# Kernel optimization log

Hardware: AMD Instinct MI355X
Metric: run time of the kernel (lower is better)

## Reference

```python
import jax, jax.numpy as jnp
from jax import lax
import numpy as np

T, D, H, E, K = 4096, 1024, 2048, 8, 2

def setup_inputs() -> dict:
    key = jax.random.key(0)
    ks = jax.random.split(key, 5)
    x = jax.random.normal(ks[0], (T, D), dtype=jnp.float32)
    weights = jax.random.uniform(ks[1], (T, K), dtype=jnp.float32)
    indices = jax.random.randint(ks[2], (T, K), 0, E, dtype=jnp.int64)
    # GatedMLP params (bias=False): fc1 weight [2H, D], fc2 weight [D, H], stacked over experts
    W1 = jax.random.normal(ks[3], (E, 2 * H, D), dtype=jnp.float32) * 0.02
    W2 = jax.random.normal(ks[4], (E, D, H), dtype=jnp.float32) * 0.02
    return {"x": x, "weights": weights, "indices": indices, "W1": W1, "W2": W2}

def reference(x, weights, indices, W1, W2):
    # Combine per-token routing weights into a per-(token, expert) weight matrix.
    # Tokens not routed to expert e get weight 0, so the dense per-expert GatedMLP
    # weighted-sum is mathematically identical to the gather->MLP->scatter-add loop.
    onehot = jax.nn.one_hot(indices, E, dtype=weights.dtype)        # [T, K, E]
    w_te = jnp.einsum('tke,tk->et', onehot, weights)                # [E, T]

    def body(y, carry):
        W1e, W2e, we = carry                                        # [2H,D], [D,H], [T]
        h = x @ W1e.T                                               # [T, 2H]
        u, gate = jnp.split(h, 2, axis=-1)                          # [T, H] each
        out = (u * jax.nn.silu(gate)) @ W2e.T                       # [T, D]
        return y + out * we[:, None], None

    y, _ = lax.scan(body, jnp.zeros_like(x), (W1, W2, w_te))
    return y
```

## Files before the change

kernel.cpp:

```cpp
#include <hip/hip_runtime.h>
#include <stdint.h>

#define T_TOK 4096
#define D_DIM 1024
#define H_DIM 2048
#define E_EXP 8
#define K_TOP 2
#define NTK   (T_TOK * K_TOP)
#define MT1 256
#define MAXT1 48

typedef short bf16x8 __attribute__((ext_vector_type(8)));
typedef float f32x4  __attribute__((ext_vector_type(4)));

#define MINI(a, b) ((a) < (b) ? (a) : (b))
#define MFMA_BF16 __builtin_amdgcn_mfma_f32_16x16x32_bf16

__device__ __forceinline__ unsigned short f2bf(float f) {
  unsigned u = __float_as_uint(f);
  u += 0x7fffu + ((u >> 16) & 1u);
  return (unsigned short)(u >> 16);
}

#define GLDS16(gp, lp)                                                        \
  __builtin_amdgcn_global_load_lds(                                           \
      (const __attribute__((address_space(1))) void*)(gp),                    \
      (__attribute__((address_space(3))) void*)(lp), 16, 0, 0)



__global__ __launch_bounds__(256) void k_route_count(const int* __restrict__ idx,
                                                     int* __restrict__ meta) {
  __shared__ int h[E_EXP];
  int tid = threadIdx.x;
  if (tid < E_EXP) h[tid] = 0;
  __syncthreads();
  int i = blockIdx.x * 256 + tid;
  atomicAdd(&h[idx[i] & (E_EXP - 1)], 1);
  __syncthreads();
  if (tid < E_EXP) atomicAdd(&meta[tid], h[tid]);
}

__global__ __launch_bounds__(64) void k_route_plan(int* __restrict__ meta) {
  if (threadIdx.x) return;
  int off = 0, nt = 0;
  for (int e = 0; e < E_EXP; ++e) {
    int c = meta[e];
    meta[8 + e]  = off;
    meta[16 + e] = off;
    for (int r = 0; r < c; r += MT1) {
      meta[32 + nt]  = e;
      meta[80 + nt]  = off + r;
      meta[128 + nt] = MINI(MT1, c - r);
      ++nt;
    }
    off += c;
  }
  meta[24] = nt;
}

__global__ __launch_bounds__(256) void k_route_scatter(const int* __restrict__ idx,
                                                       const float* __restrict__ w,
                                                       int* __restrict__ meta,
                                                       int* __restrict__ rows,
                                                       float* __restrict__ wv) {
  __shared__ int h[E_EXP], base[E_EXP];
  int tid = threadIdx.x;
  if (tid < E_EXP) h[tid] = 0;
  __syncthreads();
  int i = blockIdx.x * 256 + tid;
  int e = idx[i] & (E_EXP - 1);
  int r = atomicAdd(&h[e], 1);
  __syncthreads();
  if (tid < E_EXP) base[tid] = atomicAdd(&meta[16 + tid], h[tid]);
  __syncthreads();
  int p = base[e] + r;
  rows[p] = i >> 1;
  wv[p]   = w[i];
}

#define NX8   (T_TOK * D_DIM / 8)
#define NW18  (E_EXP * 2 * H_DIM * D_DIM / 8)
#define NW28  (E_EXP * D_DIM * H_DIM / 8)
#define NCVT8 (NX8 + NW18 + NW28)

__global__ __launch_bounds__(256) void k_cvt8(const float* __restrict__ x,
                                              const float* __restrict__ W1,
                                              const float* __restrict__ W2,
                                              unsigned short* __restrict__ xb,
                                              unsigned short* __restrict__ W1b,
                                              unsigned short* __restrict__ W2b) {
  long gid = (long)blockIdx.x * 256 + threadIdx.x;
  const float* src;
  unsigned short* dst;
  long i;
  if (gid < NX8) {
    src = x; dst = xb; i = gid;
  } else if (gid < NX8 + NW18) {
    src = W1; dst = W1b; i = gid - NX8;
  } else if (gid < NCVT8) {
    src = W2; dst = W2b; i = gid - (NX8 + NW18);
  } else return;
  float4 a = ((const float4*)src)[2 * i];
  float4 b = ((const float4*)src)[2 * i + 1];
  uint4 o;
  o.x = f2bf(a.x) | ((unsigned)f2bf(a.y) << 16);
  o.y = f2bf(a.z) | ((unsigned)f2bf(a.w) << 16);
  o.z = f2bf(b.x) | ((unsigned)f2bf(b.y) << 16);
  o.w = f2bf(b.z) | ((unsigned)f2bf(b.w) << 16);
  ((uint4*)dst)[i] = o;
}

__global__ __launch_bounds__(256, 2) void k_gemm1(
    const unsigned short* __restrict__ xb,
    const unsigned short* __restrict__ W1b,
    const int* __restrict__ meta,
    const int* __restrict__ rows,
    const float* __restrict__ wv,
    unsigned short* __restrict__ act) {
  int nt = meta[24];
  int bid = blockIdx.x;
  int xcd = bid & 7, jj = bid >> 3;
  int y   = jj & 31;
  int tb  = ((jj >> 5) << 3) + xcd;
  if (tb >= nt) return;
  int e     = meta[32 + tb];
  int r0    = meta[80 + tb];
  int valid = meta[128 + tb];
  int n0    = y << 6;

  __shared__ unsigned short lA[256 * 64];
  __shared__ unsigned short lB1[64 * 64];
  __shared__ unsigned short lB2[64 * 64];
  __shared__ float sw[256];

  int tid = threadIdx.x;
  int wave = tid >> 6, lane = tid & 63;

  sw[tid] = wv[r0 + MINI(tid, valid - 1)];

  const unsigned short* w1e = W1b + (size_t)e * (4096 * 1024);

  const unsigned short *pA[8], *pB1[2], *pB2[2];
#pragma unroll
  for (int it = 0; it < 8; ++it) {
    int c = it * 256 + tid;
    int r = c >> 3, cc = c & 7;
    int g = cc ^ (r & 7);
    int tok = rows[r0 + MINI(r, valid - 1)];
    pA[it] = xb + (size_t)tok * 1024 + g * 8;
  }
#pragma unroll
  for (int it = 0; it < 2; ++it) {
    int c = it * 256 + tid;
    int r = c >> 3, cc = c & 7;
    int g = cc ^ (r & 7);
    pB1[it] = w1e + (size_t)(n0 + r) * 1024 + g * 8;
    pB2[it] = w1e + (size_t)(2048 + n0 + r) * 1024 + g * 8;
  }

  f32x4 zero = {0.f, 0.f, 0.f, 0.f};
  f32x4 au[4][4], ag[4][4];
#pragma unroll
  for (int i = 0; i < 4; ++i)
#pragma unroll
    for (int j = 0; j < 4; ++j) { au[i][j] = zero; ag[i][j] = zero; }

  int mb = wave * 64;
  int fr = lane & 15, q = lane >> 4;

  for (int k0 = 0; k0 < 1024; k0 += 64) {
    __syncthreads();
#pragma unroll
    for (int it = 0; it < 8; ++it)
      GLDS16(pA[it] + k0, &lA[(it * 256 + wave * 64) * 8]);
#pragma unroll
    for (int it = 0; it < 2; ++it) {
      int lb = (it * 256 + wave * 64) * 8;
      GLDS16(pB1[it] + k0, &lB1[lb]);
      GLDS16(pB2[it] + k0, &lB2[lb]);
    }
    __syncthreads();
#pragma unroll
    for (int kk = 0; kk < 2; ++kk) {
      int co = (((kk << 2) + q) ^ (fr & 7)) * 8 + fr * 64;
      bf16x8 a[4];
#pragma unroll
      for (int i = 0; i < 4; ++i)
        a[i] = *(const bf16x8*)&lA[(mb + i * 16) * 64 + co];
#pragma unroll
      for (int j = 0; j < 4; ++j) {
        bf16x8 bu = *(const bf16x8*)&lB1[(j * 16) * 64 + co];
        bf16x8 bg = *(const bf16x8*)&lB2[(j * 16) * 64 + co];
#pragma unroll
        for (int i = 0; i < 4; ++i) {
          au[i][j] = MFMA_BF16(a[i], bu, au[i][j], 0, 0, 0);
          ag[i][j] = MFMA_BF16(a[i], bg, ag[i][j], 0, 0, 0);
        }
      }
    }
  }

#pragma unroll
  for (int i = 0; i < 4; ++i) {
#pragma unroll
    for (int reg = 0; reg < 4; ++reg) {
      int lm = mb + i * 16 + q * 4 + reg;
      if (lm < valid) {
        float wrow = sw[lm];
        size_t orow = (size_t)(r0 + lm) * 2048;
#pragma unroll
        for (int j = 0; j < 4; ++j) {
          float u = au[i][j][reg];
          float g = ag[i][j][reg];
          float s = g / (1.f + __expf(-g));
          act[orow + (n0 + j * 16 + fr)] = f2bf(u * s * wrow);
        }
      }
    }
  }
}

__global__ __launch_bounds__(256, 2) void k_gemm2(
    const unsigned short* __restrict__ act,
    const unsigned short* __restrict__ W2b,
    const int* __restrict__ meta,
    const int* __restrict__ rows,
    float* __restrict__ out) {
  int nt = meta[24];
  int bid = blockIdx.x;
  int xcd = bid & 7, jj = bid >> 3;
  int y   = jj & 7;
  int tb  = ((jj >> 3) << 3) + xcd;
  if (tb >= nt) return;
  int e     = meta[32 + tb];
  int r0    = meta[80 + tb];
  int valid = meta[128 + tb];
  int n0    = y << 7;

  __shared__ unsigned short lA[256 * 64];
  __shared__ unsigned short lB[128 * 64];
  __shared__ int st[256];

  int tid = threadIdx.x;
  int wave = tid >> 6, lane = tid & 63;
  st[tid] = rows[r0 + MINI(tid, valid - 1)];

  const unsigned short* w2e = W2b + (size_t)e * (1024 * 2048);

  const unsigned short *pA[8], *pB[4];
#pragma unroll
  for (int it = 0; it < 8; ++it) {
    int c = it * 256 + tid;
    int r = c >> 3, cc = c & 7;
    int g = cc ^ (r & 7);
    pA[it] = act + (size_t)(r0 + MINI(r, valid - 1)) * 2048 + g * 8;
  }
#pragma unroll
  for (int it = 0; it < 4; ++it) {
    int c = it * 256 + tid;
    int r = c >> 3, cc = c & 7;
    int g = cc ^ (r & 7);
    pB[it] = w2e + (size_t)(n0 + r) * 2048 + g * 8;
  }

  f32x4 zero = {0.f, 0.f, 0.f, 0.f};
  f32x4 acc[4][8];
#pragma unroll
  for (int i = 0; i < 4; ++i)
#pragma unroll
    for (int j = 0; j < 8; ++j) acc[i][j] = zero;

  int mb = wave * 64;
  int fr = lane & 15, q = lane >> 4;

  for (int k0 = 0; k0 < 2048; k0 += 64) {
    __syncthreads();
#pragma unroll
    for (int it = 0; it < 8; ++it)
      GLDS16(pA[it] + k0, &lA[(it * 256 + wave * 64) * 8]);
#pragma unroll
    for (int it = 0; it < 4; ++it)
      GLDS16(pB[it] + k0, &lB[(it * 256 + wave * 64) * 8]);
    __syncthreads();
#pragma unroll
    for (int kk = 0; kk < 2; ++kk) {
      int co = (((kk << 2) + q) ^ (fr & 7)) * 8 + fr * 64;
      bf16x8 a[4];
#pragma unroll
      for (int i = 0; i < 4; ++i)
        a[i] = *(const bf16x8*)&lA[(mb + i * 16) * 64 + co];
#pragma unroll
      for (int j = 0; j < 8; ++j) {
        bf16x8 b = *(const bf16x8*)&lB[(j * 16) * 64 + co];
#pragma unroll
        for (int i = 0; i < 4; ++i)
          acc[i][j] = MFMA_BF16(a[i], b, acc[i][j], 0, 0, 0);
      }
    }
  }

#pragma unroll
  for (int i = 0; i < 4; ++i) {
#pragma unroll
    for (int reg = 0; reg < 4; ++reg) {
      int lm = mb + i * 16 + q * 4 + reg;
      if (lm < valid) {
        int tok = st[lm];
        float* op = out + (size_t)tok * 1024;
#pragma unroll
        for (int j = 0; j < 8; ++j)
          atomicAdd(&op[n0 + j * 16 + fr], acc[i][j][reg]);
      }
    }
  }
}

extern "C" void kernel_launch(void* const* d_in, const int* in_sizes, int n_in,
                              void* d_out, int out_size, void* d_ws, size_t ws_size,
                              hipStream_t stream) {
  const float* x  = (const float*)d_in[0];
  const float* w  = (const float*)d_in[1];
  const int*  idx = (const int*)d_in[2];
  const float* W1 = (const float*)d_in[3];
  const float* W2 = (const float*)d_in[4];
  float* out = (float*)d_out;

  char* ws = (char*)d_ws;
  unsigned short* W1b = (unsigned short*)(ws);
  unsigned short* W2b = (unsigned short*)(ws + 67108864);
  unsigned short* xb  = (unsigned short*)(ws + 100663296);
  unsigned short* act = (unsigned short*)(ws + 109051904);
  int*   rows = (int*)(ws + 142606336);
  float* wv   = (float*)(ws + 142639104);
  int*   meta = (int*)(ws + 142671872);

  hipMemsetAsync(d_out, 0, (size_t)out_size * sizeof(float), stream);
  hipMemsetAsync(meta, 0, 1024, stream);

  k_cvt8<<<(NCVT8 + 255) / 256, 256, 0, stream>>>(x, W1, W2, xb, W1b, W2b);
  k_route_count<<<32, 256, 0, stream>>>(idx, meta);
  k_route_plan<<<1, 64, 0, stream>>>(meta);
  k_route_scatter<<<32, 256, 0, stream>>>(idx, w, meta, rows, wv);

  k_gemm1<<<MAXT1 * 32, 256, 0, stream>>>(xb, W1b, meta, rows, wv, act);
  k_gemm2<<<MAXT1 * 8, 256, 0, stream>>>(act, W2b, meta, rows, out);
}
```

Before: 460.6 us.

## Overlap W2 conversion and output zeroing with gemm1; fuse route count into cvt

Result: faster. 423.0 us (-8.2%).

```diff
diff --git a/kernel.cpp b/kernel.cpp
--- a/kernel.cpp
+++ b/kernel.cpp
@@ -28,17 +28,44 @@
       (__attribute__((address_space(3))) void*)(lp), 16, 0, 0)
 
 
-
-__global__ __launch_bounds__(256) void k_route_count(const int* __restrict__ idx,
-                                                     int* __restrict__ meta) {
-  __shared__ int h[E_EXP];
+#define NX8   (T_TOK * D_DIM / 8)
+#define NW18  (E_EXP * 2 * H_DIM * D_DIM / 8)
+#define NW28  (E_EXP * D_DIM * H_DIM / 8)
+#define PRE_CVT_BLKS ((NX8 + NW18) / 256)
+#define PRE_BLKS (PRE_CVT_BLKS + 32)
+
+__global__ __launch_bounds__(256) void k_pre(const float* __restrict__ x,
+                                             const float* __restrict__ W1,
+                                             const int* __restrict__ idx,
+                                             unsigned short* __restrict__ xb,
+                                             unsigned short* __restrict__ W1b,
+                                             int* __restrict__ meta) {
+  int bid = blockIdx.x;
   int tid = threadIdx.x;
-  if (tid < E_EXP) h[tid] = 0;
-  __syncthreads();
-  int i = blockIdx.x * 256 + tid;
-  atomicAdd(&h[idx[i] & (E_EXP - 1)], 1);
-  __syncthreads();
-  if (tid < E_EXP) atomicAdd(&meta[tid], h[tid]);
+  if (bid >= PRE_CVT_BLKS) {
+    __shared__ int h[E_EXP];
+    if (tid < E_EXP) h[tid] = 0;
+    __syncthreads();
+    int i = (bid - PRE_CVT_BLKS) * 256 + tid;
+    atomicAdd(&h[idx[i] & (E_EXP - 1)], 1);
+    __syncthreads();
+    if (tid < E_EXP) atomicAdd(&meta[tid], h[tid]);
+    return;
+  }
+  long gid = (long)bid * 256 + tid;
+  const float* src;
+  unsigned short* dst;
+  long i;
+  if (gid < NX8) { src = x; dst = xb; i = gid; }
+  else           { src = W1; dst = W1b; i = gid - NX8; }
+  float4 a = ((const float4*)src)[2 * i];
+  float4 b = ((const float4*)src)[2 * i + 1];
+  uint4 o;
+  o.x = f2bf(a.x) | ((unsigned)f2bf(a.y) << 16);
+  o.y = f2bf(a.z) | ((unsigned)f2bf(a.w) << 16);
+  o.z = f2bf(b.x) | ((unsigned)f2bf(b.y) << 16);
+  o.w = f2bf(b.z) | ((unsigned)f2bf(b.w) << 16);
+  ((uint4*)dst)[i] = o;
 }
 
 __global__ __launch_bounds__(64) void k_route_plan(int* __restrict__ meta) {
@@ -79,37 +106,10 @@
   wv[p]   = w[i];
 }
 
-#define NX8   (T_TOK * D_DIM / 8)
-#define NW18  (E_EXP * 2 * H_DIM * D_DIM / 8)
-#define NW28  (E_EXP * D_DIM * H_DIM / 8)
-#define NCVT8 (NX8 + NW18 + NW28)
-
-__global__ __launch_bounds__(256) void k_cvt8(const float* __restrict__ x,
-                                              const float* __restrict__ W1,
-                                              const float* __restrict__ W2,
-                                              unsigned short* __restrict__ xb,
-                                              unsigned short* __restrict__ W1b,
-                                              unsigned short* __restrict__ W2b) {
-  long gid = (long)blockIdx.x * 256 + threadIdx.x;
-  const float* src;
-  unsigned short* dst;
-  long i;
-  if (gid < NX8) {
-    src = x; dst = xb; i = gid;
-  } else if (gid < NX8 + NW18) {
-    src = W1; dst = W1b; i = gid - NX8;
-  } else if (gid < NCVT8) {
-    src = W2; dst = W2b; i = gid - (NX8 + NW18);
-  } else return;
-  float4 a = ((const float4*)src)[2 * i];
-  float4 b = ((const float4*)src)[2 * i + 1];
-  uint4 o;
-  o.x = f2bf(a.x) | ((unsigned)f2bf(a.y) << 16);
-  o.y = f2bf(a.z) | ((unsigned)f2bf(a.w) << 16);
-  o.z = f2bf(b.x) | ((unsigned)f2bf(b.y) << 16);
-  o.w = f2bf(b.z) | ((unsigned)f2bf(b.w) << 16);
-  ((uint4*)dst)[i] = o;
-}
+#define G1_TILES (MAXT1 * 32)
+#define CVW2_BLK 1024
+#define ZOUT_BLK 64
+#define G1_GRID  (G1_TILES + CVW2_BLK + ZOUT_BLK)
 
 __global__ __launch_bounds__(256, 2) void k_gemm1(
     const unsigned short* __restrict__ xb,
@@ -117,12 +117,40 @@
     const int* __restrict__ meta,
     const int* __restrict__ rows,
     const float* __restrict__ wv,
-    unsigned short* __restrict__ act) {
+    unsigned short* __restrict__ act,
+    const float* __restrict__ W2,
+    unsigned short* __restrict__ W2b,
+    float* __restrict__ out) {
+  int bid = blockIdx.x;
+  int tid = threadIdx.x;
+
+  if (bid >= G1_TILES) {
+    int xb2 = bid - G1_TILES;
+    if (xb2 < CVW2_BLK) {
+      long g0 = (long)xb2 * 256 + tid;
+      for (long i = g0; i < NW28; i += (long)CVW2_BLK * 256) {
+        float4 a = ((const float4*)W2)[2 * i];
+        float4 b = ((const float4*)W2)[2 * i + 1];
+        uint4 o;
+        o.x = f2bf(a.x) | ((unsigned)f2bf(a.y) << 16);
+        o.y = f2bf(a.z) | ((unsigned)f2bf(a.w) << 16);
+        o.z = f2bf(b.x) | ((unsigned)f2bf(b.y) << 16);
+        o.w = f2bf(b.z) | ((unsigned)f2bf(b.w) << 16);
+        ((uint4*)W2b)[i] = o;
+      }
+    } else {
+      int zb = xb2 - CVW2_BLK;
+      long g0 = (long)zb * 256 + tid;
+      uint4 z = {0u, 0u, 0u, 0u};
+      for (long i = g0; i < (long)(T_TOK * D_DIM / 4); i += (long)ZOUT_BLK * 256)
+        ((uint4*)out)[i] = z;
+    }
+    return;
+  }
+
   int nt = meta[24];
-  int bid = blockIdx.x;
-  int xcd = bid & 7, jj = bid >> 3;
-  int y   = jj & 31;
-  int tb  = ((jj >> 5) << 3) + xcd;
+  int tb = bid % MAXT1;
+  int y  = bid / MAXT1;
   if (tb >= nt) return;
   int e     = meta[32 + tb];
   int r0    = meta[80 + tb];
@@ -134,7 +162,6 @@
   __shared__ unsigned short lB2[64 * 64];
   __shared__ float sw[256];
 
-  int tid = threadIdx.x;
   int wave = tid >> 6, lane = tid & 63;
 
   sw[tid] = wv[r0 + MINI(tid, valid - 1)];
@@ -228,15 +255,12 @@
     const int* __restrict__ rows,
     float* __restrict__ out) {
   int nt = meta[24];
-  int bid = blockIdx.x;
-  int xcd = bid & 7, jj = bid >> 3;
-  int y   = jj & 7;
-  int tb  = ((jj >> 3) << 3) + xcd;
+  int tb = blockIdx.x;
   if (tb >= nt) return;
   int e     = meta[32 + tb];
   int r0    = meta[80 + tb];
   int valid = meta[128 + tb];
-  int n0    = y << 7;
+  int n0    = blockIdx.y * 128;
 
   __shared__ unsigned short lA[256 * 64];
   __shared__ unsigned short lB[128 * 64];
@@ -335,14 +359,15 @@
   float* wv   = (float*)(ws + 142639104);
   int*   meta = (int*)(ws + 142671872);
 
-  hipMemsetAsync(d_out, 0, (size_t)out_size * sizeof(float), stream);
   hipMemsetAsync(meta, 0, 1024, stream);
 
-  k_cvt8<<<(NCVT8 + 255) / 256, 256, 0, stream>>>(x, W1, W2, xb, W1b, W2b);
-  k_route_count<<<32, 256, 0, stream>>>(idx, meta);
+  k_pre<<<PRE_BLKS, 256, 0, stream>>>(x, W1, idx, xb, W1b, meta);
   k_route_plan<<<1, 64, 0, stream>>>(meta);
   k_route_scatter<<<32, 256, 0, stream>>>(idx, w, meta, rows, wv);
 
-  k_gemm1<<<MAXT1 * 32, 256, 0, stream>>>(xb, W1b, meta, rows, wv, act);
-  k_gemm2<<<MAXT1 * 8, 256, 0, stream>>>(act, W2b, meta, rows, out);
-}
+  k_gemm1<<<G1_GRID, 256, 0, stream>>>(xb, W1b, meta, rows, wv, act,
+                                       W2, W2b, out);
+
+  dim3 g2(MAXT1, D_DIM / 128);
+  k_gemm2<<<g2, 256, 0, stream>>>(act, W2b, meta, rows, out);
+}
```
